# Performance work log

Hardware: AMD Instinct MI355X
Metric: run time of the kernel (lower is better)

Reference implementation:

```python
import jax, jax.numpy as jnp
import numpy as np

B, T = 32, 2048
STATE, ACT, LAT, ENC = 128, 16, 256, 1024  # input_dim = STATE + 2*ACT = 160


def setup_inputs() -> dict:
    key = jax.random.key(0)
    ks = jax.random.split(key, 16)
    s = lambda k, shp, sc=0.05: jax.random.normal(k, shp, dtype=jnp.float32) * sc
    return {
        "padded_input": jax.random.normal(ks[0], (B, T, STATE + 2 * ACT), dtype=jnp.float32),
        "enc_w1": s(ks[1], (STATE, ENC)), "enc_b1": s(ks[2], (ENC,)),
        "enc_w2": s(ks[3], (ENC, ENC)),   "enc_b2": s(ks[4], (ENC,)),
        "enc_w3": s(ks[5], (ENC, LAT)),   "enc_b3": s(ks[6], (LAT,)),
        "a_diag": jax.random.uniform(ks[7], (LAT,), minval=-0.8, maxval=0.8, dtype=jnp.float32),
        "B_w": s(ks[8], (ACT, LAT)),
        "dec_w1": s(ks[9], (LAT, ENC)),  "dec_b1": s(ks[10], (ENC,)),
        "dec_w2": s(ks[11], (ENC, ENC)), "dec_b2": s(ks[12], (ENC,)),
        "dec_w3": s(ks[13], (ENC, STATE)), "dec_b3": s(ks[14], (STATE,)),
        "nwarmup": 4,
    }


def reference(padded_input, enc_w1, enc_b1, enc_w2, enc_b2, enc_w3, enc_b3,
              a_diag, B_w, dec_w1, dec_b1, dec_w2, dec_b2, dec_w3, dec_b3,
              nwarmup):
    # slice state / actuator channels
    x_t = padded_input[:, :, :STATE]                      # [B,T,STATE]
    u_t1 = padded_input[:, :, STATE + ACT:]               # [B,T,ACT]

    def encoder(x):
        h = jnp.tanh(x @ enc_w1 + enc_b1)
        h = jnp.tanh(h @ enc_w2 + enc_b2)
        return jnp.tanh(h @ enc_w3 + enc_b3)

    def decoder(z):
        h = jnp.tanh(z @ dec_w1 + dec_b1)
        h = jnp.tanh(h @ dec_w2 + dec_b2)
        return h @ dec_w3 + dec_b3

    z_t = encoder(x_t)                                    # [B,T,LAT]
    a = jnp.clip(a_diag, -0.95, 0.95)                     # clamped diagonal of A
    Bu = u_t1 @ B_w                                       # [B,T,LAT]

    # diagonal linear recurrence with warmup resets (reset_probability=0)
    zT = jnp.swapaxes(z_t, 0, 1)                          # [T,B,LAT]
    BuT = jnp.swapaxes(Bu, 0, 1)                          # [T,B,LAT]
    ts = jnp.arange(T)

    def step(prev, inputs):
        z, bu, t = inputs
        inp = jnp.where(t <= nwarmup, z, prev)
        out = a * inp + bu
        return out, out

    _, outs = jax.lax.scan(step, z_t[:, 0, :], (zT, BuT, ts))
    z_t1 = jnp.swapaxes(outs, 0, 1)                       # [B,T,LAT]
    return decoder(z_t1)                                  # [B,T,STATE]
```

## Files before the change

kernel.cpp:

```cpp
#include <hip/hip_runtime.h>
#include <stdint.h>
#include <type_traits>

#define B_ 32
#define T_ 2048
#define STATE_ 128
#define ACT_ 16
#define LAT_ 256
#define ENC_ 1024
#define ROWS_ (B_ * T_)
#define TENC_ 16
#define MENC_ (B_ * TENC_)
#define NCHUNK_ 64
#define LCHUNK_ 32
#define SLAB_ 32768

using bf16x8 = __attribute__((ext_vector_type(8))) short;
using f32x4  = __attribute__((ext_vector_type(4))) float;
using f32x16 = __attribute__((ext_vector_type(16))) float;

__device__ __forceinline__ uint16_t f2bf(float f) {
  uint32_t u = __float_as_uint(f);
  u += 0x7fff + ((u >> 16) & 1);
  return (uint16_t)(u >> 16);
}

__device__ __forceinline__ float fast_tanh(float x) {
  float e = __expf(2.f * x);
  return 1.f - 2.f / (e + 1.f);
}

__device__ __forceinline__ void xcd_remap(int gx, int gy, int& bm, int& bn) {
  if (((gy & 7) == 0) && ((gx & (gx - 1)) == 0)) {
    const int lin  = blockIdx.y * gx + blockIdx.x;
    const int xcd  = lin & 7;
    const int slot = lin >> 3;
    const int lgx  = 31 - __clz(gx);
    bn = slot & (gx - 1);
    bm = ((slot >> lgx) << 3) + xcd;
  } else {
    bm = blockIdx.y;
    bn = blockIdx.x;
  }
}

template <bool TANH, typename OUT_T>
__device__ __forceinline__ void store4(OUT_T* C, size_t m, int N, int nb,
                                       const float* bias, f32x4 a) {
  const float4 bv = *(const float4*)(bias + nb);
  float v0 = a[0] + bv.x, v1 = a[1] + bv.y, v2 = a[2] + bv.z, v3 = a[3] + bv.w;
  if (TANH) {
    v0 = fast_tanh(v0); v1 = fast_tanh(v1);
    v2 = fast_tanh(v2); v3 = fast_tanh(v3);
  }
  if constexpr (std::is_same<OUT_T, uint16_t>::value) {
    uint32_t p0 = (uint32_t)f2bf(v0) | ((uint32_t)f2bf(v1) << 16);
    uint32_t p1 = (uint32_t)f2bf(v2) | ((uint32_t)f2bf(v3) << 16);
    uint2 p = {p0, p1};
    *(uint2*)(C + m * N + nb) = p;
  } else {
    float4 p = {v0, v1, v2, v3};
    *(float4*)(C + m * N + nb) = p;
  }
}

template <bool TANH, typename OUT_T>
__global__ __launch_bounds__(256) void gemm_bt(
    const uint16_t* __restrict__ A, const uint16_t* __restrict__ Bt,
    const float* __restrict__ bias, OUT_T* __restrict__ C,
    int M, int N, int K) {
  __shared__ uint16_t smA[128 * 64];
  __shared__ uint16_t smB[128 * 64];
  const int tid  = threadIdx.x;
  const int lane = tid & 63;
  const int wave = tid >> 6;
  const int wm = wave >> 1, wn = wave & 1;
  const int l32 = lane & 31, h = lane >> 5;

  int bm, bn;
  xcd_remap(gridDim.x, gridDim.y, bm, bn);
  const int m0 = bm * 128;
  const int n0 = bn * 128;

  const int srow = wave * 32 + (lane >> 3);
  const int sblk = lane & 7;

  f32x16 acc[2][2];
#pragma unroll
  for (int i = 0; i < 2; ++i)
#pragma unroll
    for (int j = 0; j < 2; ++j)
#pragma unroll
      for (int r = 0; r < 16; ++r) acc[i][j][r] = 0.f;

  for (int k0 = 0; k0 < K; k0 += 64) {
#pragma unroll
    for (int i = 0; i < 4; ++i) {
      const int r  = srow + i * 8;
      const int kb = sblk ^ (r & 7);
      const uint16_t* ga = A  + (size_t)(m0 + r) * K + (k0 + kb * 8);
      const uint16_t* gb = Bt + (size_t)(n0 + r) * K + (k0 + kb * 8);
      uint16_t* la = smA + (size_t)(wave * 32 + i * 8) * 64;
      uint16_t* lb = smB + (size_t)(wave * 32 + i * 8) * 64;
      __builtin_amdgcn_global_load_lds(
          (const __attribute__((address_space(1))) void*)ga,
          (__attribute__((address_space(3))) void*)la, 16, 0, 0);
      __builtin_amdgcn_global_load_lds(
          (const __attribute__((address_space(1))) void*)gb,
          (__attribute__((address_space(3))) void*)lb, 16, 0, 0);
    }
    __syncthreads();

#pragma unroll
    for (int ks = 0; ks < 4; ++ks) {
      bf16x8 af[2], bfr[2];
      const int kslot = ks * 2 + h;
#pragma unroll
      for (int mt = 0; mt < 2; ++mt) {
        const int row  = wm * 64 + mt * 32 + l32;
        const int slot = kslot ^ (row & 7);
        af[mt] = *(const bf16x8*)(smA + (size_t)row * 64 + slot * 8);
      }
#pragma unroll
      for (int nt = 0; nt < 2; ++nt) {
        const int row  = wn * 64 + nt * 32 + l32;
        const int slot = kslot ^ (row & 7);
        bfr[nt] = *(const bf16x8*)(smB + (size_t)row * 64 + slot * 8);
      }
#pragma unroll
      for (int mt = 0; mt < 2; ++mt)
#pragma unroll
        for (int nt = 0; nt < 2; ++nt)
          acc[mt][nt] = __builtin_amdgcn_mfma_f32_32x32x16_bf16(
              bfr[nt], af[mt], acc[mt][nt], 0, 0, 0);
    }
    __syncthreads();
  }

#pragma unroll
  for (int mt = 0; mt < 2; ++mt) {
    const size_t m = m0 + wm * 64 + mt * 32 + l32;
#pragma unroll
    for (int nt = 0; nt < 2; ++nt) {
#pragma unroll
      for (int q = 0; q < 4; ++q) {
        const int nb = n0 + wn * 64 + nt * 32 + q * 8 + h * 4;
        f32x4 v = {acc[mt][nt][4 * q + 0], acc[mt][nt][4 * q + 1],
                   acc[mt][nt][4 * q + 2], acc[mt][nt][4 * q + 3]};
        store4<TANH>(C, m, N, nb, bias, v);
      }
    }
  }
}

template <bool TANH, typename OUT_T>
__global__ __launch_bounds__(256, 2) void gemm_wide(
    const uint16_t* __restrict__ A, const uint16_t* __restrict__ Bt,
    const float* __restrict__ bias, OUT_T* __restrict__ C,
    int M, int N, int K) {
  __shared__ uint16_t smA[128 * 64];
  __shared__ uint16_t smB[256 * 64];
  const int tid  = threadIdx.x;
  const int lane = tid & 63;
  const int wave = tid >> 6;
  const int wm = wave >> 1, wn = wave & 1;
  const int l32 = lane & 31, h = lane >> 5;

  int bm, bn;
  xcd_remap(gridDim.x, gridDim.y, bm, bn);
  const int m0 = bm * 128;
  const int n0 = bn * 256;

  const int sr8  = lane >> 3;
  const int sblk = lane & 7;

  f32x16 acc[2][4];
#pragma unroll
  for (int i = 0; i < 2; ++i)
#pragma unroll
    for (int j = 0; j < 4; ++j)
#pragma unroll
      for (int r = 0; r < 16; ++r) acc[i][j][r] = 0.f;

  for (int k0 = 0; k0 < K; k0 += 64) {
#pragma unroll
    for (int i = 0; i < 4; ++i) {
      const int r  = wave * 32 + sr8 + i * 8;
      const int kb = sblk ^ (r & 7);
      const uint16_t* ga = A + (size_t)(m0 + r) * K + (k0 + kb * 8);
      uint16_t* la = smA + (size_t)r * 64;
      __builtin_amdgcn_global_load_lds(
          (const __attribute__((address_space(1))) void*)ga,
          (__attribute__((address_space(3))) void*)la, 16, 0, 0);
    }
#pragma unroll
    for (int i = 0; i < 8; ++i) {
      const int r  = wave * 64 + sr8 + i * 8;
      const int kb = sblk ^ (r & 7);
      const uint16_t* gb = Bt + (size_t)(n0 + r) * K + (k0 + kb * 8);
      uint16_t* lb = smB + (size_t)r * 64;
      __builtin_amdgcn_global_load_lds(
          (const __attribute__((address_space(1))) void*)gb,
          (__attribute__((address_space(3))) void*)lb, 16, 0, 0);
    }
    __syncthreads();

#pragma unroll
    for (int ks = 0; ks < 4; ++ks) {
      bf16x8 af[2], bfr[4];
      const int kslot = ks * 2 + h;
#pragma unroll
      for (int mt = 0; mt < 2; ++mt) {
        const int row  = wm * 64 + mt * 32 + l32;
        const int slot = kslot ^ (row & 7);
        af[mt] = *(const bf16x8*)(smA + (size_t)row * 64 + slot * 8);
      }
#pragma unroll
      for (int nt = 0; nt < 4; ++nt) {
        const int row  = wn * 128 + nt * 32 + l32;
        const int slot = kslot ^ (row & 7);
        bfr[nt] = *(const bf16x8*)(smB + (size_t)row * 64 + slot * 8);
      }
#pragma unroll
      for (int mt = 0; mt < 2; ++mt)
#pragma unroll
        for (int nt = 0; nt < 4; ++nt)
          acc[mt][nt] = __builtin_amdgcn_mfma_f32_32x32x16_bf16(
              bfr[nt], af[mt], acc[mt][nt], 0, 0, 0);
    }
    __syncthreads();
  }

#pragma unroll
  for (int mt = 0; mt < 2; ++mt) {
    const size_t m = m0 + wm * 64 + mt * 32 + l32;
#pragma unroll
    for (int nt = 0; nt < 4; ++nt) {
#pragma unroll
      for (int q = 0; q < 4; ++q) {
        const int nb = n0 + wn * 128 + nt * 32 + q * 8 + h * 4;
        f32x4 v = {acc[mt][nt][4 * q + 0], acc[mt][nt][4 * q + 1],
                   acc[mt][nt][4 * q + 2], acc[mt][nt][4 * q + 3]};
        store4<TANH>(C, m, N, nb, bias, v);
      }
    }
  }
}

template <bool TANH, typename OUT_T>
__global__ __launch_bounds__(512, 2) void gemm256(
    const uint16_t* A, const uint16_t* __restrict__ Bt,
    const float* __restrict__ bias, OUT_T* C,
    int M, int N, int K) {
  __shared__ uint16_t smA[2 * 2 * 128 * 64];
  __shared__ uint16_t smB[2 * 2 * 128 * 64];
  const int tid  = threadIdx.x;
  const int l    = tid & 63;
  const int wv   = tid >> 6;
  const int wm   = wv >> 2;
  const int wn   = wv & 3;
  const int lr   = l & 15, quad = l >> 4;
  const int x7   = lr & 7;

  int bm, bn;
  xcd_remap(gridDim.x, gridDim.y, bm, bn);
  const int m0 = bm * 256;
  const int n0 = bn * 256;

  const int jr0 = wv * 16 + (l >> 3);
  const int kbe = ((l & 7) ^ (l >> 3)) * 8;
  int garow[2], gbrow[2];
#pragma unroll
  for (int i = 0; i < 2; ++i) {
    const int jr = jr0 + i * 8;
    garow[i] = (jr & 63) + ((jr >> 6) * 128);
    gbrow[i] = (jr & 31) + ((jr >> 5) * 64);
  }
  const int NT = K >> 6;

  const int arow = wm * 64 + lr;
  const int brow = wn * 32 + lr;

  f32x4 acc[8][4];
#pragma unroll
  for (int i = 0; i < 8; ++i)
#pragma unroll
    for (int j = 0; j < 4; ++j) acc[i][j] = f32x4{0.f, 0.f, 0.f, 0.f};

  bf16x8 af[4][2];
  bf16x8 bf0[2][2];
  bf16x8 bf1[2][2];

  auto stA = [&](int t, int h, int par) {
#pragma unroll
    for (int i = 0; i < 2; ++i) {
      const uint16_t* g =
          A + (size_t)(m0 + garow[i] + h * 64) * K + (t * 64 + kbe);
      uint16_t* d = smA + (size_t)((par * 2 + h) * 128 + wv * 16 + i * 8) * 64;
      __builtin_amdgcn_global_load_lds(
          (const __attribute__((address_space(1))) void*)g,
          (__attribute__((address_space(3))) void*)d, 16, 0, 0);
    }
  };
  auto stB = [&](int t, int h, int par) {
#pragma unroll
    for (int i = 0; i < 2; ++i) {
      const uint16_t* g =
          Bt + (size_t)(n0 + gbrow[i] + h * 32) * K + (t * 64 + kbe);
      uint16_t* d = smB + (size_t)((par * 2 + h) * 128 + wv * 16 + i * 8) * 64;
      __builtin_amdgcn_global_load_lds(
          (const __attribute__((address_space(1))) void*)g,
          (__attribute__((address_space(3))) void*)d, 16, 0, 0);
    }
  };
  auto ldA = [&](int rh, int par) {
#pragma unroll
    for (int f = 0; f < 4; ++f)
#pragma unroll
      for (int ks = 0; ks < 2; ++ks)
        af[f][ks] = *(const bf16x8*)(smA +
            (size_t)((par * 2 + rh) * 128 + arow + f * 16) * 64 +
            ((ks * 4 + quad) ^ x7) * 8);
  };
  auto ldB = [&](int ch, int par, bf16x8 (&dst)[2][2]) {
#pragma unroll
    for (int c2 = 0; c2 < 2; ++c2)
#pragma unroll
      for (int ks = 0; ks < 2; ++ks)
        dst[c2][ks] = *(const bf16x8*)(smB +
            (size_t)((par * 2 + ch) * 128 + brow + c2 * 16) * 64 +
            ((ks * 4 + quad) ^ x7) * 8);
  };
  auto mm = [&](int rh, int ch, bf16x8 (&bfr)[2][2]) {
#pragma unroll
    for (int ks = 0; ks < 2; ++ks)
#pragma unroll
      for (int f = 0; f < 4; ++f)
#pragma unroll
        for (int c2 = 0; c2 < 2; ++c2)
          acc[rh * 4 + f][ch * 2 + c2] =
              __builtin_amdgcn_mfma_f32_16x16x32_bf16(
                  bfr[c2][ks], af[f][ks], acc[rh * 4 + f][ch * 2 + c2],
                  0, 0, 0);
  };

#define BARRIER() asm volatile("s_barrier" ::: "memory")
#define WLGKM0()  asm volatile("s_waitcnt lgkmcnt(0)" ::: "memory")

  stA(0, 0, 0); stB(0, 0, 0); stB(0, 1, 0); stA(0, 1, 0);
  if (NT > 1) { stA(1, 0, 1); stB(1, 0, 1); stB(1, 1, 1); }
  asm volatile("s_waitcnt vmcnt(6)" ::: "memory");
  BARRIER();

  auto window = [&](int w, int par) {
    ldA(0, par);
    ldB(0, par, bf0);
    if (w + 1 < NT) stA(w + 1, 1, par ^ 1);
    BARRIER(); WLGKM0();
    __builtin_amdgcn_s_setprio(1); mm(0, 0, bf0); __builtin_amdgcn_s_setprio(0);
    BARRIER();
    ldB(1, par, bf1);
    if (w + 2 < NT) stA(w + 2, 0, par);
    BARRIER(); WLGKM0();
    __builtin_amdgcn_s_setprio(1); mm(0, 1, bf1); __builtin_amdgcn_s_setprio(0);
    BARRIER();
    ldA(1, par);
    if (w + 2 < NT) stB(w + 2, 0, par);
    BARRIER(); WLGKM0();
    __builtin_amdgcn_s_setprio(1); mm(1, 1, bf1); __builtin_amdgcn_s_setprio(0);
    BARRIER();
    if (w + 2 < NT) stB(w + 2, 1, par);
    __builtin_amdgcn_s_setprio(1); mm(1, 0, bf0); __builtin_amdgcn_s_setprio(0);
    if (w + 2 < NT) asm volatile("s_waitcnt vmcnt(6)" ::: "memory");
    else            asm volatile("s_waitcnt vmcnt(0)" ::: "memory");
    BARRIER();
  };

  for (int w = 0; w < NT; w += 2) {
    window(w, 0);
    window(w + 1, 1);
  }

#undef BARRIER
#undef WLGKM0

#pragma unroll
  for (int rf = 0; rf < 8; ++rf) {
    const size_t m = m0 + wm * 128 + rf * 16 + lr;
#pragma unroll
    for (int cf = 0; cf < 4; ++cf) {
      const int nb = n0 + wn * 64 + cf * 16 + quad * 4;
      store4<TANH>(C, m, N, nb, bias, acc[rf][cf]);
    }
  }
}

template <bool TANH, typename OUT_T>
__global__ __launch_bounds__(256) void gemm64(
    const uint16_t* __restrict__ A, const uint16_t* __restrict__ Bt,
    const float* __restrict__ bias, OUT_T* __restrict__ C,
    int M, int N, int K) {
  __shared__ uint16_t smA[64 * 64];
  __shared__ uint16_t smB[128 * 64];
  const int tid  = threadIdx.x;
  const int lane = tid & 63;
  const int wave = tid >> 6;
  const int wm = wave >> 1, wn = wave & 1;
  const int lr = lane & 15, quad = lane >> 4;

  int bm, bn;
  xcd_remap(gridDim.x, gridDim.y, bm, bn);
  const int m0 = bm * 64;
  const int n0 = bn * 128;

  const int sr8  = lane >> 3;
  const int sblk = lane & 7;

  f32x4 vzero = {0.f, 0.f, 0.f, 0.f};
  f32x4 acc[2][4];
#pragma unroll
  for (int i = 0; i < 2; ++i)
#pragma unroll
    for (int j = 0; j < 4; ++j) acc[i][j] = vzero;

  for (int k0 = 0; k0 < K; k0 += 64) {
#pragma unroll
    for (int i = 0; i < 2; ++i) {
      const int r  = wave * 16 + sr8 + i * 8;
      const int kb = sblk ^ (r & 7);
      const uint16_t* ga = A + (size_t)(m0 + r) * K + (k0 + kb * 8);
      uint16_t* la = smA + (size_t)r * 64;
      __builtin_amdgcn_global_load_lds(
          (const __attribute__((address_space(1))) void*)ga,
          (__attribute__((address_space(3))) void*)la, 16, 0, 0);
    }
#pragma unroll
    for (int i = 0; i < 4; ++i) {
      const int r  = wave * 32 + sr8 + i * 8;
      const int kb = sblk ^ (r & 7);
      const uint16_t* gb = Bt + (size_t)(n0 + r) * K + (k0 + kb * 8);
      uint16_t* lb = smB + (size_t)r * 64;
      __builtin_amdgcn_global_load_lds(
          (const __attribute__((address_space(1))) void*)gb,
          (__attribute__((address_space(3))) void*)lb, 16, 0, 0);
    }
    __syncthreads();

#pragma unroll
    for (int ks = 0; ks < 2; ++ks) {
      bf16x8 af[2], bfr[4];
      const int slotx = (ks * 4 + quad);
#pragma unroll
      for (int mt = 0; mt < 2; ++mt) {
        const int row  = wm * 32 + mt * 16 + lr;
        const int slot = slotx ^ (lr & 7);
        af[mt] = *(const bf16x8*)(smA + (size_t)row * 64 + slot * 8);
      }
#pragma unroll
      for (int nt = 0; nt < 4; ++nt) {
        const int row  = wn * 64 + nt * 16 + lr;
        const int slot = slotx ^ (lr & 7);
        bfr[nt] = *(const bf16x8*)(smB + (size_t)row * 64 + slot * 8);
      }
#pragma unroll
      for (int mt = 0; mt < 2; ++mt)
#pragma unroll
        for (int nt = 0; nt < 4; ++nt)
          acc[mt][nt] = __builtin_amdgcn_mfma_f32_16x16x32_bf16(
              bfr[nt], af[mt], acc[mt][nt], 0, 0, 0);
    }
    __syncthreads();
  }

#pragma unroll
  for (int mt = 0; mt < 2; ++mt) {
    const size_t m = m0 + wm * 32 + mt * 16 + lr;
#pragma unroll
    for (int nt = 0; nt < 4; ++nt) {
      const int nb = n0 + wn * 64 + nt * 16 + quad * 4;
      store4<TANH>(C, m, N, nb, bias, acc[mt][nt]);
    }
  }
}

struct TArgs {
  const float* s[6];
  uint16_t* d[6];
  int R[6];
  int C[6];
  const float* pin;
  uint16_t* xc;
};

__global__ __launch_bounds__(256) void transpose_cast(TArgs a) {
  const int z = blockIdx.z;
  if (z == 6) {
    const int idx = (blockIdx.y * 32 + blockIdx.x) * 256 + threadIdx.x;
    if (idx < MENC_ * STATE_) {
      const int r = idx >> 7, c = idx & 127;
      const int b = r / TENC_, t = r % TENC_;
      a.xc[idx] = f2bf(a.pin[((size_t)b * T_ + t) * 160 + c]);
    }
    return;
  }
  __shared__ float tile[32][33];
  const float* s = a.s[z];
  uint16_t* d = a.d[z];
  const int R = a.R[z], C = a.C[z];
  const int bc = blockIdx.x * 32, br = blockIdx.y * 32;
  if (bc >= C || br >= R) return;
  const int tx = threadIdx.x & 31, ty = threadIdx.x >> 5;
#pragma unroll
  for (int i = 0; i < 32; i += 8)
    tile[ty + i][tx] = s[(size_t)(br + ty + i) * C + (bc + tx)];
  __syncthreads();
#pragma unroll
  for (int i = 0; i < 32; i += 8)
    d[(size_t)(bc + ty + i) * R + (br + tx)] = f2bf(tile[tx][ty + i]);
}

__device__ __forceinline__ float clip_a(const float* a_diag, int l) {
  return fminf(fmaxf(a_diag[l], -0.95f), 0.95f);
}

__device__ __forceinline__ float bu_at(const float* __restrict__ pin, int b,
                                       int t, const float* bw) {
  const float* u = pin + ((size_t)b * T_ + t) * 160 + 144;
  float bu = 0.f;
#pragma unroll
  for (int k = 0; k < ACT_; ++k) bu += u[k] * bw[k];
  return bu;
}

__global__ __launch_bounds__(256) void rec_pass1(
    const float* __restrict__ Zc, const float* __restrict__ pin,
    const float* __restrict__ Bw, const float* __restrict__ a_diag,
    const int* __restrict__ nwp, float* __restrict__ F) {
  const int l = threadIdx.x, c = blockIdx.x, b = blockIdx.y;
  const int nw = *nwp;
  const float a = clip_a(a_diag, l);
  float bw[ACT_];
#pragma unroll
  for (int k = 0; k < ACT_; ++k) bw[k] = Bw[k * LAT_ + l];

  float s = (c == 0) ? Zc[(size_t)b * TENC_ * LAT_ + l] : 0.f;
  const int t0 = c * LCHUNK_;
  for (int j = 0; j < LCHUNK_; ++j) {
    const int t = t0 + j;
    float inp;
    if (t <= nw) {
      const int tt = t < TENC_ ? t : TENC_ - 1;
      inp = Zc[((size_t)b * TENC_ + tt) * LAT_ + l];
    } else {
      inp = s;
    }
    s = a * inp + bu_at(pin, b, t, bw);
  }
  F[((size_t)c * B_ + b) * LAT_ + l] = s;
}

__global__ __launch_bounds__(256) void rec_pass3(
    const float* __restrict__ Zc, const float* __restrict__ pin,
    const float* __restrict__ Bw, const float* __restrict__ a_diag,
    const int* __restrict__ nwp, const float* __restrict__ F,
    uint16_t* __restrict__ Zp) {
  const int l = threadIdx.x, c = blockIdx.x, b = blockIdx.y;
  const int nw = *nwp;
  const float a = clip_a(a_diag, l);
  float bw[ACT_];
#pragma unroll
  for (int k = 0; k < ACT_; ++k) bw[k] = Bw[k * LAT_ + l];

  float aL = a;
#pragma unroll
  for (int i = 0; i < 5; ++i) aL *= aL;
  float s = Zc[(size_t)b * TENC_ * LAT_ + l];
  for (int cc = 1; cc <= c; ++cc) {
    const float Fp = F[((size_t)(cc - 1) * B_ + b) * LAT_ + l];
    const bool exact = ((cc - 1) == 0) || (nw >= (cc - 1) * LCHUNK_);
    s = exact ? Fp : (aL * s + Fp);
  }

  const int t0 = c * LCHUNK_;
  for (int j = 0; j < LCHUNK_; ++j) {
    const int t = t0 + j;
    float inp;
    if (t <= nw) {
      const int tt = t < TENC_ ? t : TENC_ - 1;
      inp = Zc[((size_t)b * TENC_ + tt) * LAT_ + l];
    } else {
      inp = s;
    }
    s = a * inp + bu_at(pin, b, t, bw);
    Zp[((size_t)b * T_ + t) * LAT_ + l] = f2bf(s);
  }
}

extern "C" void kernel_launch(void* const* d_in, const int* in_sizes, int n_in,
                              void* d_out, int out_size, void* d_ws,
                              size_t ws_size, hipStream_t stream) {
  const float* pin = (const float*)d_in[0];
  const float* ew1 = (const float*)d_in[1];
  const float* eb1 = (const float*)d_in[2];
  const float* ew2 = (const float*)d_in[3];
  const float* eb2 = (const float*)d_in[4];
  const float* ew3 = (const float*)d_in[5];
  const float* eb3 = (const float*)d_in[6];
  const float* adg = (const float*)d_in[7];
  const float* Bw  = (const float*)d_in[8];
  const float* dw1 = (const float*)d_in[9];
  const float* db1 = (const float*)d_in[10];
  const float* dw2 = (const float*)d_in[11];
  const float* db2 = (const float*)d_in[12];
  const float* dw3 = (const float*)d_in[13];
  const float* db3 = (const float*)d_in[14];
  const int* nwp   = (const int*)d_in[15];
  float* out = (float*)d_out;

  uint8_t* ws = (uint8_t*)d_ws;
  size_t off = 0;
  auto alloc = [&](size_t b) -> void* {
    void* p = ws + off;
    off += (b + 255) & ~(size_t)255;
    return p;
  };
  uint16_t* W1t = (uint16_t*)alloc((size_t)ENC_ * STATE_ * 2);
  uint16_t* W2t = (uint16_t*)alloc((size_t)ENC_ * ENC_ * 2);
  uint16_t* W3t = (uint16_t*)alloc((size_t)LAT_ * ENC_ * 2);
  uint16_t* D1t = (uint16_t*)alloc((size_t)ENC_ * LAT_ * 2);
  uint16_t* D2t = (uint16_t*)alloc((size_t)ENC_ * ENC_ * 2);
  uint16_t* D3t = (uint16_t*)alloc((size_t)STATE_ * ENC_ * 2);
  uint16_t* Xc  = (uint16_t*)alloc((size_t)MENC_ * STATE_ * 2);
  float* Zc = (float*)alloc((size_t)MENC_ * LAT_ * 4);
  float* F  = (float*)alloc((size_t)NCHUNK_ * B_ * LAT_ * 4);
  uint16_t* Zp = (uint16_t*)alloc((size_t)ROWS_ * LAT_ * 2);

  const size_t full_g = (size_t)ROWS_ * ENC_ * 2;
  int slab_rows, nslab;
  size_t g_bytes;
  if (ws_size >= off + full_g + 256) {
    slab_rows = ROWS_;  nslab = 1;  g_bytes = full_g;
  } else {
    slab_rows = SLAB_;  nslab = 2;  g_bytes = (size_t)SLAB_ * ENC_ * 2;
  }
  uint16_t* G = (uint16_t*)alloc(g_bytes);
  uint16_t* H1c = G;
  uint16_t* H2c = G + (size_t)MENC_ * ENC_;

  if (ws_size < off) return;

  TArgs ta;
  ta.s[0] = ew1; ta.d[0] = W1t; ta.R[0] = STATE_; ta.C[0] = ENC_;
  ta.s[1] = ew2; ta.d[1] = W2t; ta.R[1] = ENC_;   ta.C[1] = ENC_;
  ta.s[2] = ew3; ta.d[2] = W3t; ta.R[2] = ENC_;   ta.C[2] = LAT_;
  ta.s[3] = dw1; ta.d[3] = D1t; ta.R[3] = LAT_;   ta.C[3] = ENC_;
  ta.s[4] = dw2; ta.d[4] = D2t; ta.R[4] = ENC_;   ta.C[4] = ENC_;
  ta.s[5] = dw3; ta.d[5] = D3t; ta.R[5] = ENC_;   ta.C[5] = STATE_;
  ta.pin = pin;  ta.xc = Xc;
  transpose_cast<<<dim3(32, 32, 7), 256, 0, stream>>>(ta);

  gemm_bt<true, uint16_t><<<dim3(ENC_ / 128, MENC_ / 128), 256, 0, stream>>>(
      Xc, W1t, eb1, H1c, MENC_, ENC_, STATE_);
  gemm_bt<true, uint16_t><<<dim3(ENC_ / 128, MENC_ / 128), 256, 0, stream>>>(
      H1c, W2t, eb2, H2c, MENC_, ENC_, ENC_);
  gemm64<true, float><<<dim3(LAT_ / 128, MENC_ / 64), 256, 0, stream>>>(
      H2c, W3t, eb3, Zc, MENC_, LAT_, ENC_);

  rec_pass1<<<dim3(NCHUNK_, B_), 256, 0, stream>>>(Zc, pin, Bw, adg, nwp, F);
  rec_pass3<<<dim3(NCHUNK_, B_), 256, 0, stream>>>(Zc, pin, Bw, adg, nwp, F,
                                                   Zp);

  for (int s = 0; s < nslab; ++s) {
    const uint16_t* Zs = Zp + (size_t)s * slab_rows * LAT_;
    float* Os = out + (size_t)s * slab_rows * STATE_;
    gemm_wide<true, uint16_t><<<dim3(ENC_ / 256, slab_rows / 128), 256, 0,
                                stream>>>(Zs, D1t, db1, G, slab_rows, ENC_,
                                          LAT_);
    gemm256<true, uint16_t><<<dim3(ENC_ / 256, slab_rows / 256), 512, 0,
                              stream>>>(G, D2t, db2, G, slab_rows, ENC_,
                                        ENC_);
    gemm_bt<false, float><<<dim3(STATE_ / 128, slab_rows / 128), 256, 0,
                            stream>>>(G, D3t, db3, Os, slab_rows, STATE_,
                                      ENC_);
  }
}
```

Measured before the change: 488.6 us.

## Make decoder gemm256 process multiple M tiles per block with continuous pipeline

The 1024x1024 decoder GEMM kernel now walks several consecutive 256-row M tiles per block. It flattens (tile, k-step) into one software-pipelined loop, so global-to-LDS prefetch carries across tile boundaries. Accumulators are stored with bias and tanh at each tile end and then reset. The launch grid is fixed at 64 row-blocks, which halves the block count. That trades per-block pipeline prologue and drain for fewer resident blocks, which may lower latency hiding.

Measured after the change: 486.1 us. No clear change (-0.5%).

```diff
diff --git a/kernel.cpp b/kernel.cpp
--- a/kernel.cpp
+++ b/kernel.cpp
@@ -264,8 +264,12 @@
 
   int bm, bn;
   xcd_remap(gridDim.x, gridDim.y, bm, bn);
-  const int m0 = bm * 256;
   const int n0 = bn * 256;
+
+  const int NT  = K >> 6;
+  const int tpb = (M >> 8) / gridDim.y;
+  const int W   = tpb * NT;
+  const int mt0 = bm * tpb;
 
   const int jr0 = wv * 16 + (l >> 3);
   const int kbe = ((l & 7) ^ (l >> 3)) * 8;
@@ -276,7 +280,6 @@
     garow[i] = (jr & 63) + ((jr >> 6) * 128);
     gbrow[i] = (jr & 31) + ((jr >> 5) * 64);
   }
-  const int NT = K >> 6;
 
   const int arow = wm * 64 + lr;
   const int brow = wn * 32 + lr;
@@ -291,22 +294,26 @@
   bf16x8 bf0[2][2];
   bf16x8 bf1[2][2];
 
-  auto stA = [&](int t, int h, int par) {
+  auto stA = [&](int wt, int h, int par) {
+    const int tile = wt / NT, kt = wt - tile * NT;
+    const int m0t = (mt0 + tile) << 8;
 #pragma unroll
     for (int i = 0; i < 2; ++i) {
       const uint16_t* g =
-          A + (size_t)(m0 + garow[i] + h * 64) * K + (t * 64 + kbe);
+          A + (size_t)(m0t + garow[i] + h * 64) * K + (kt * 64 + kbe);
       uint16_t* d = smA + (size_t)((par * 2 + h) * 128 + wv * 16 + i * 8) * 64;
       __builtin_amdgcn_global_load_lds(
           (const __attribute__((address_space(1))) void*)g,
           (__attribute__((address_space(3))) void*)d, 16, 0, 0);
     }
   };
-  auto stB = [&](int t, int h, int par) {
+  auto stB = [&](int wt, int h, int par) {
+    const int tile = wt / NT, kt = wt - tile * NT;
+    (void)tile;
 #pragma unroll
     for (int i = 0; i < 2; ++i) {
       const uint16_t* g =
-          Bt + (size_t)(n0 + gbrow[i] + h * 32) * K + (t * 64 + kbe);
+          Bt + (size_t)(n0 + gbrow[i] + h * 32) * K + (kt * 64 + kbe);
       uint16_t* d = smB + (size_t)((par * 2 + h) * 128 + wv * 16 + i * 8) * 64;
       __builtin_amdgcn_global_load_lds(
           (const __attribute__((address_space(1))) void*)g,
@@ -348,51 +355,57 @@
 #define WLGKM0()  asm volatile("s_waitcnt lgkmcnt(0)" ::: "memory")
 
   stA(0, 0, 0); stB(0, 0, 0); stB(0, 1, 0); stA(0, 1, 0);
-  if (NT > 1) { stA(1, 0, 1); stB(1, 0, 1); stB(1, 1, 1); }
+  if (W > 1) { stA(1, 0, 1); stB(1, 0, 1); stB(1, 1, 1); }
   asm volatile("s_waitcnt vmcnt(6)" ::: "memory");
   BARRIER();
 
   auto window = [&](int w, int par) {
     ldA(0, par);
     ldB(0, par, bf0);
-    if (w + 1 < NT) stA(w + 1, 1, par ^ 1);
+    if (w + 1 < W) stA(w + 1, 1, par ^ 1);
     BARRIER(); WLGKM0();
     __builtin_amdgcn_s_setprio(1); mm(0, 0, bf0); __builtin_amdgcn_s_setprio(0);
     BARRIER();
     ldB(1, par, bf1);
-    if (w + 2 < NT) stA(w + 2, 0, par);
+    if (w + 2 < W) stA(w + 2, 0, par);
     BARRIER(); WLGKM0();
     __builtin_amdgcn_s_setprio(1); mm(0, 1, bf1); __builtin_amdgcn_s_setprio(0);
     BARRIER();
     ldA(1, par);
-    if (w + 2 < NT) stB(w + 2, 0, par);
+    if (w + 2 < W) stB(w + 2, 0, par);
     BARRIER(); WLGKM0();
     __builtin_amdgcn_s_setprio(1); mm(1, 1, bf1); __builtin_amdgcn_s_setprio(0);
     BARRIER();
-    if (w + 2 < NT) stB(w + 2, 1, par);
+    if (w + 2 < W) stB(w + 2, 1, par);
     __builtin_amdgcn_s_setprio(1); mm(1, 0, bf0); __builtin_amdgcn_s_setprio(0);
-    if (w + 2 < NT) asm volatile("s_waitcnt vmcnt(6)" ::: "memory");
-    else            asm volatile("s_waitcnt vmcnt(0)" ::: "memory");
+    if (w + 2 < W) asm volatile("s_waitcnt vmcnt(6)" ::: "memory");
+    else           asm volatile("s_waitcnt vmcnt(0)" ::: "memory");
     BARRIER();
   };
 
-  for (int w = 0; w < NT; w += 2) {
+  for (int w = 0; w < W; w += 2) {
     window(w, 0);
     window(w + 1, 1);
+    if ((w + 1) % NT == NT - 1) {
+      const int m0s = (mt0 + (w + 1) / NT) << 8;
+#pragma unroll
+      for (int rf = 0; rf < 8; ++rf) {
+        const size_t m = m0s + wm * 128 + rf * 16 + lr;
+#pragma unroll
+        for (int cf = 0; cf < 4; ++cf) {
+          const int nb = n0 + wn * 64 + cf * 16 + quad * 4;
+          store4<TANH>(C, m, N, nb, bias, acc[rf][cf]);
+        }
+      }
+#pragma unroll
+      for (int i = 0; i < 8; ++i)
+#pragma unroll
+        for (int j = 0; j < 4; ++j) acc[i][j] = f32x4{0.f, 0.f, 0.f, 0.f};
+    }
   }
 
 #undef BARRIER
 #undef WLGKM0
-
-#pragma unroll
-  for (int rf = 0; rf < 8; ++rf) {
-    const size_t m = m0 + wm * 128 + rf * 16 + lr;
-#pragma unroll
-    for (int cf = 0; cf < 4; ++cf) {
-      const int nb = n0 + wn * 64 + cf * 16 + quad * 4;
-      store4<TANH>(C, m, N, nb, bias, acc[rf][cf]);
-    }
-  }
 }
 
 template <bool TANH, typename OUT_T>
@@ -676,7 +689,7 @@
     gemm_wide<true, uint16_t><<<dim3(ENC_ / 256, slab_rows / 128), 256, 0,
                                 stream>>>(Zs, D1t, db1, G, slab_rows, ENC_,
                                           LAT_);
-    gemm256<true, uint16_t><<<dim3(ENC_ / 256, slab_rows / 256), 512, 0,
+    gemm256<true, uint16_t><<<dim3(ENC_ / 256, 64), 512, 0,
                               stream>>>(G, D2t, db2, G, slab_rows, ENC_,
                                         ENC_);
     gemm_bt<false, float><<<dim3(STATE_ / 128, slab_rows / 128), 256, 0,
```
